# Optimization experiments

Hardware: AMD Instinct MI355X
Metric: run time of the kernel (lower is better)

The kernel has to match this reference:

```python
import jax, jax.numpy as jnp
import numpy as np

B, S, MD, H = 8, 1024, 1024, 16
D = MD // H  # 64
# Faithful to torch: scale = (dim_per_head // num_heads) ** -0.5 (a quirk, not 1/sqrt(D))
SCALE = float((D // H) ** (-0.5))


def setup_inputs() -> dict:
    k0 = jax.random.key(0)
    ks = jax.random.split(k0, 11)
    w = 1.0 / np.sqrt(MD)
    mk = lambda k, shape, s: jax.random.normal(k, shape, dtype=jnp.float32) * s
    return {
        "query": mk(ks[0], (B, S, MD), 1.0),
        "key": mk(ks[1], (B, S, MD), 1.0),
        "value": mk(ks[2], (B, S, MD), 1.0),
        "Wq": mk(ks[3], (MD, MD), w), "bq": mk(ks[4], (MD,), w),
        "Wk": mk(ks[5], (MD, MD), w), "bk": mk(ks[6], (MD,), w),
        "Wv": mk(ks[7], (MD, MD), w), "bv": mk(ks[8], (MD,), w),
        "Wo": mk(ks[9], (MD, MD), w), "bo": mk(ks[10], (MD,), w),
    }


def reference(query, key, value, Wq, bq, Wk, bk, Wv, bv, Wo, bo):
    # Dropout is identity in eval mode (deterministic reference).
    Bq, T, _ = query.shape
    Sk = key.shape[1]
    q = query @ Wq + bq   # [B, T, H*D]
    k = key @ Wk + bk     # [B, S, H*D]
    v = value @ Wv + bv
    # Faithful replication of torch .view(B*H, -1, D): plain row-major reshape
    # (NOT a head transpose -- it chunks sequence/head indices together).
    q = q.reshape(Bq * H, T, D)
    k = k.reshape(Bq * H, Sk, D)
    v = v.reshape(Bq * H, Sk, D)
    attn = jnp.einsum('btd,bsd->bts', q, k) * SCALE          # [B*H, T, S]
    p = jax.nn.softmax(attn, axis=-1)
    ctx = jnp.einsum('bts,bsd->btd', p, v).reshape(Bq, T, H * D)
    output = ctx @ Wo + bo                                    # [B, T, MD]
    a = attn.reshape(Bq, H, T, Sk)
    attn_post = jax.nn.sigmoid(a).sum(axis=1) / H             # [B, T, S]
    return output, attn_post
```

## Files before the change

### kernel.cpp

```cpp
#include <hip/hip_runtime.h>


typedef __attribute__((ext_vector_type(8))) short bf16x8;
typedef __attribute__((ext_vector_type(4))) float f32x4;

static __device__ __forceinline__ short f2bf(float f) {
  union { float f; unsigned u; } v; v.f = f;
  unsigned lsb = (v.u >> 16) & 1u;
  v.u += 0x7fffu + lsb;
  return (short)(v.u >> 16);
}

static __device__ __forceinline__ short f2bf_rhu(float f) {
  union { float f; unsigned u; } v; v.f = f;
  v.u += 0x8000u;
  return (short)(v.u >> 16);
}

static __device__ __forceinline__ float exp2_hw(float x) {
  float r;
  asm("v_exp_f32 %0, %1" : "=v"(r) : "v"(x));
  return r;
}

#define L2E_HALF 0.72134752f

#define GLDS16(gp, lp) __builtin_amdgcn_global_load_lds( \
    (const __attribute__((address_space(1))) void*)(gp), \
    (__attribute__((address_space(3))) void*)(lp), 16, 0, 0)

struct Ptr4 { const float* s[4]; short* d[4]; };
struct Ptr3 { const float* s[3]; short* d[3]; };
struct QkvArgs { const short* A[3]; const short* B[3]; const float* bias[3]; short* C[3]; };

__global__ __launch_bounds__(256) void convt4(Ptr4 a)
{
  const float* __restrict__ src = a.s[blockIdx.z];
  short* __restrict__ dst = a.d[blockIdx.z];
  __shared__ float T[64][65];
  const int tid = threadIdx.x;
  const int c0 = blockIdx.x * 64, r0 = blockIdx.y * 64;
  {
    const int rr = tid >> 4, cc = (tid & 15) * 4;
    for (int i = 0; i < 4; ++i) {
      int row = rr + i * 16;
      const float4 v = *(const float4*)(src + (size_t)(r0 + row) * 1024 + c0 + cc);
      T[row][cc] = v.x; T[row][cc + 1] = v.y; T[row][cc + 2] = v.z; T[row][cc + 3] = v.w;
    }
  }
  __syncthreads();
  {
    const int rr = tid >> 3, cc = (tid & 7) * 8;
    for (int i = 0; i < 2; ++i) {
      int row = rr + i * 32;
      bf16x8 v;
      for (int j = 0; j < 8; ++j) v[j] = f2bf(T[cc + j][row]);
      *(bf16x8*)(dst + (size_t)(c0 + row) * 1024 + r0 + cc) = v;
    }
  }
}

__global__ __launch_bounds__(256) void cvt3(Ptr3 a)
{
  const float* __restrict__ src = a.s[blockIdx.z];
  short* __restrict__ dst = a.d[blockIdx.z];
  const size_t i = ((size_t)blockIdx.x * 256 + threadIdx.x) * 8;
  const float4 v0 = *(const float4*)(src + i);
  const float4 v1 = *(const float4*)(src + i + 4);
  bf16x8 o;
  o[0] = f2bf(v0.x); o[1] = f2bf(v0.y); o[2] = f2bf(v0.z); o[3] = f2bf(v0.w);
  o[4] = f2bf(v1.x); o[5] = f2bf(v1.y); o[6] = f2bf(v1.z); o[7] = f2bf(v1.w);
  *(bf16x8*)(dst + i) = o;
}

__global__ __launch_bounds__(256) void transp_v(
    const short* __restrict__ src, short* __restrict__ dst)
{
  __shared__ short T[64][72];
  const int g = blockIdx.y, t0 = blockIdx.x * 64;
  const short* s = src + (size_t)g * 65536 + (size_t)t0 * 64;
  short* d = dst + (size_t)g * 65536 + t0;
  const int r = threadIdx.x >> 3, c = (threadIdx.x & 7) * 8;
  for (int i = 0; i < 2; ++i) {
    bf16x8 v = *(const bf16x8*)(s + (size_t)(r + i * 32) * 64 + c);
    *(bf16x8*)(&T[r + i * 32][c]) = v;
  }
  __syncthreads();
  for (int i = 0; i < 2; ++i) {
    int dr = r + i * 32;
    bf16x8 v;
    for (int j = 0; j < 8; ++j) v[j] = T[c + j][dr];
    *(bf16x8*)(d + (size_t)dr * 1024 + c) = v;
  }
}

static __device__ __forceinline__ void gemm_body(
    const short* __restrict__ A, const short* __restrict__ BT,
    const float* __restrict__ bias, void* __restrict__ Cp, int mode)
{
  __shared__ short As[128 * 64];
  __shared__ short Bs[128 * 64];
  const int K = 1024, N = 1024;
  const int tid = threadIdx.x;
  const int lane = tid & 63, wave = tid >> 6;
  const int quad = lane >> 4, l16 = lane & 15;
  const int wm = (wave & 1) * 64, wn = (wave >> 1) * 64;
  const int bm = blockIdx.x * 128, bn = blockIdx.y * 128;

  f32x4 acc[4][4] = {};

  const int s_row = tid >> 3;
  const int s_col = (tid & 7) * 8;
  const int lds_base = wave * 512;

  for (int k0 = 0; k0 < K; k0 += 64) {
    for (int i = 0; i < 4; ++i) {
      int row = s_row + i * 32;
      GLDS16(A + (size_t)(bm + row) * K + k0 + s_col, &As[i * 2048 + lds_base]);
      GLDS16(BT + (size_t)(bn + row) * K + k0 + s_col, &Bs[i * 2048 + lds_base]);
    }
    __syncthreads();
    for (int ks = 0; ks < 2; ++ks) {
      bf16x8 af[4], bfr[4];
      for (int mi = 0; mi < 4; ++mi)
        af[mi] = *(const bf16x8*)(&As[(wm + mi * 16 + l16) * 64 + ks * 32 + quad * 8]);
      for (int ni = 0; ni < 4; ++ni)
        bfr[ni] = *(const bf16x8*)(&Bs[(wn + ni * 16 + l16) * 64 + ks * 32 + quad * 8]);
      for (int mi = 0; mi < 4; ++mi)
        for (int ni = 0; ni < 4; ++ni)
          acc[mi][ni] = __builtin_amdgcn_mfma_f32_16x16x32_bf16(af[mi], bfr[ni], acc[mi][ni], 0, 0, 0);
    }
    __syncthreads();
  }

  for (int ni = 0; ni < 4; ++ni) {
    int col = bn + wn + ni * 16 + l16;
    float bv = bias[col];
    for (int mi = 0; mi < 4; ++mi) {
      int row0 = bm + wm + mi * 16 + quad * 4;
      for (int r = 0; r < 4; ++r) {
        int row = row0 + r;
        float fv = acc[mi][ni][r] + bv;
        if (mode == 2) ((float*)Cp)[(size_t)row * N + col] = fv;
        else           ((short*)Cp)[(size_t)row * N + col] = f2bf(fv);
      }
    }
  }
}

__global__ __launch_bounds__(256) void gemm_bt16(
    const short* __restrict__ A, const short* __restrict__ BT,
    const float* __restrict__ bias, void* __restrict__ Cp, int mode)
{
  gemm_body(A, BT, bias, Cp, mode);
}

__global__ __launch_bounds__(256) void gemm_qkv(QkvArgs a)
{
  const int z = blockIdx.z;
  gemm_body(a.A[z], a.B[z], a.bias[z], a.C[z], 0);
}

__global__ __launch_bounds__(256) void attn_fused6(
    const short* __restrict__ Qp, const short* __restrict__ Kp,
    const short* __restrict__ VpT,
    short* __restrict__ ctx,
    float* __restrict__ attn_post)
{
  __shared__ short Plds[16][1032];
  __shared__ float red[16][4];
  __shared__ float ctxred[4][16][64];

  const int tid = threadIdx.x;
  const int wave = tid >> 6, lane = tid & 63;
  const int quad = lane >> 4, l16 = lane & 15;
  const int orig = blockIdx.x;
  const int b = orig & 7;
  const int t0 = (orig >> 3) * 16;
  const int sbase = wave * 256;

  float sig[16][4] = {};

  for (int h = 0; h < 16; ++h) {
    const int g = b * 16 + h;
    const short* Qg = Qp + (size_t)g * 65536;
    const short* Kg = Kp + (size_t)g * 65536;
    const short* Vg = VpT + (size_t)g * 65536;

    bf16x8 aq0 = *(const bf16x8*)(Qg + (t0 + l16) * 64 + quad * 8);
    bf16x8 aq1 = *(const bf16x8*)(Qg + (t0 + l16) * 64 + 32 + quad * 8);

    float sc[16][4];
    float rsum[4] = {0.f, 0.f, 0.f, 0.f};

    bf16x8 kb0[4], kb1[4];
#pragma unroll
    for (int t = 0; t < 4; ++t) {
      int s = sbase + t * 16;
      kb0[t] = *(const bf16x8*)(Kg + (s + l16) * 64 + quad * 8);
      kb1[t] = *(const bf16x8*)(Kg + (s + l16) * 64 + 32 + quad * 8);
    }
#pragma unroll
    for (int tile = 0; tile < 16; ++tile) {
      const int slot = tile & 3;
      bf16x8 bk0 = kb0[slot], bk1 = kb1[slot];
      if (tile < 12) {
        int s = sbase + (tile + 4) * 16;
        kb0[slot] = *(const bf16x8*)(Kg + (s + l16) * 64 + quad * 8);
        kb1[slot] = *(const bf16x8*)(Kg + (s + l16) * 64 + 32 + quad * 8);
      }
      f32x4 c = {0.f, 0.f, 0.f, 0.f};
      c = __builtin_amdgcn_mfma_f32_16x16x32_bf16(aq0, bk0, c, 0, 0, 0);
      c = __builtin_amdgcn_mfma_f32_16x16x32_bf16(aq1, bk1, c, 0, 0, 0);
#pragma unroll
      for (int r = 0; r < 4; ++r) {
        float e = exp2_hw(c[r] * L2E_HALF);
        sc[tile][r] = e;
        rsum[r] += e;
        sig[tile][r] += e * __builtin_amdgcn_rcpf(1.f + e);
      }
    }
#pragma unroll
    for (int r = 0; r < 4; ++r)
      for (int mask = 1; mask < 16; mask <<= 1) rsum[r] += __shfl_xor(rsum[r], mask, 64);
    if (l16 == 0)
      for (int r = 0; r < 4; ++r) red[quad * 4 + r][wave] = rsum[r];
    __syncthreads();
#pragma unroll
    for (int r = 0; r < 4; ++r) {
      int row = quad * 4 + r;
      float s4 = red[row][0] + red[row][1] + red[row][2] + red[row][3];
      float inv = __builtin_amdgcn_rcpf(s4);
#pragma unroll
      for (int tile = 0; tile < 16; ++tile)
        Plds[row][sbase + tile * 16 + l16] = f2bf_rhu(sc[tile][r] * inv);
    }

    f32x4 cacc[4] = {};
    bf16x8 apb[2], vb[2][4];
    apb[0] = *(const bf16x8*)(&Plds[l16][sbase + quad * 8]);
#pragma unroll
    for (int ni = 0; ni < 4; ++ni)
      vb[0][ni] = *(const bf16x8*)(Vg + (ni * 16 + l16) * 1024 + sbase + quad * 8);
#pragma unroll
    for (int ks = 0; ks < 8; ++ks) {
      const int cur = ks & 1, nxt = cur ^ 1;
      if (ks < 7) {
        apb[nxt] = *(const bf16x8*)(&Plds[l16][sbase + (ks + 1) * 32 + quad * 8]);
#pragma unroll
        for (int ni = 0; ni < 4; ++ni)
          vb[nxt][ni] = *(const bf16x8*)(Vg + (ni * 16 + l16) * 1024 + sbase + (ks + 1) * 32 + quad * 8);
      }
#pragma unroll
      for (int ni = 0; ni < 4; ++ni)
        cacc[ni] = __builtin_amdgcn_mfma_f32_16x16x32_bf16(apb[cur], vb[cur][ni], cacc[ni], 0, 0, 0);
    }

    for (int ni = 0; ni < 4; ++ni)
      for (int r = 0; r < 4; ++r)
        ctxred[wave][quad * 4 + r][ni * 16 + l16] = cacc[ni][r];
    __syncthreads();
    short* ctxg = ctx + (size_t)g * 65536 + t0 * 64;
    for (int e = tid; e < 1024; e += 256) {
      int t = e >> 6, dd = e & 63;
      float v = ctxred[0][t][dd] + ctxred[1][t][dd] + ctxred[2][t][dd] + ctxred[3][t][dd];
      ctxg[t * 64 + dd] = f2bf(v);
    }
  }

  float* ap_out = attn_post + (size_t)b * 1048576 + (size_t)t0 * 1024;
  for (int tile = 0; tile < 16; ++tile)
    for (int r = 0; r < 4; ++r)
      ap_out[(quad * 4 + r) * 1024 + sbase + tile * 16 + l16] = sig[tile][r] * 0.0625f;
}

extern "C" void kernel_launch(void* const* d_in, const int* in_sizes, int n_in,
                              void* d_out, int out_size, void* d_ws, size_t ws_size,
                              hipStream_t stream) {
  const float* query = (const float*)d_in[0];
  const float* key   = (const float*)d_in[1];
  const float* value = (const float*)d_in[2];
  const float* Wq = (const float*)d_in[3]; const float* bq = (const float*)d_in[4];
  const float* Wk = (const float*)d_in[5]; const float* bk = (const float*)d_in[6];
  const float* Wv = (const float*)d_in[7]; const float* bv = (const float*)d_in[8];
  const float* Wo = (const float*)d_in[9]; const float* bo = (const float*)d_in[10];

  float* out0 = (float*)d_out;
  float* attn_post = out0 + (8u << 20);

  short* WqT = (short*)d_ws;
  short* WkT = WqT + (1u << 20);
  short* WvT = WkT + (1u << 20);
  short* WoT = WvT + (1u << 20);
  short* Qp  = WoT + (1u << 20);
  short* Kp  = Qp + (8u << 20);
  short* VpT = Kp + (8u << 20);

  dim3 blk(256);
  const size_t NEED_BIG = (size_t)(60u << 20) * 2;

  convt4<<<dim3(16, 16, 4), blk, 0, stream>>>(
      Ptr4{{Wq, Wk, Wv, Wo}, {WqT, WkT, WvT, WoT}});

  short* ctx;
  if (ws_size >= NEED_BIG) {
    short* Xq = VpT + (8u << 20);
    short* Xk = Xq + (8u << 20);
    short* Xv = Xk + (8u << 20);
    short* Vflat = Xv + (8u << 20);
    ctx = Xq;

    cvt3<<<dim3(4096, 1, 3), blk, 0, stream>>>(Ptr3{{query, key, value}, {Xq, Xk, Xv}});
    gemm_qkv<<<dim3(64, 8, 3), blk, 0, stream>>>(
        QkvArgs{{Xq, Xk, Xv}, {WqT, WkT, WvT}, {bq, bk, bv}, {Qp, Kp, Vflat}});
    transp_v<<<dim3(16, 128), blk, 0, stream>>>(Vflat, VpT);
  } else {
    short* Xin = VpT + (8u << 20);
    short* Vflat = Xin + (8u << 20);
    ctx = Xin;

    cvt3<<<dim3(4096, 1, 1), blk, 0, stream>>>(Ptr3{{query, query, query}, {Xin, Xin, Xin}});
    gemm_bt16<<<dim3(64, 8), blk, 0, stream>>>(Xin, WqT, bq, Qp, 0);
    cvt3<<<dim3(4096, 1, 1), blk, 0, stream>>>(Ptr3{{key, key, key}, {Xin, Xin, Xin}});
    gemm_bt16<<<dim3(64, 8), blk, 0, stream>>>(Xin, WkT, bk, Kp, 0);
    cvt3<<<dim3(4096, 1, 1), blk, 0, stream>>>(Ptr3{{value, value, value}, {Xin, Xin, Xin}});
    gemm_bt16<<<dim3(64, 8), blk, 0, stream>>>(Xin, WvT, bv, Vflat, 0);
    transp_v<<<dim3(16, 128), blk, 0, stream>>>(Vflat, VpT);
  }

  attn_fused6<<<dim3(512), blk, 0, stream>>>(Qp, Kp, VpT, ctx, attn_post);
  gemm_bt16<<<dim3(64, 8), blk, 0, stream>>>(ctx, WoT, bo, out0, 2);
}
```

Baseline: 526.7 us.

## Split PV matmul by head-dim across waves, defer softmax normalization

Each wave now computes a 16-column slice of the head dimension over the full key length, instead of a partial sum over a quarter of the keys. This removes the ctxred shared-memory cross-wave reduction and its extra pass. Unnormalized exponentials are written straight into LDS during the score loop, so the sc register array is gone, and the row-sum reciprocal is applied to the context afterwards. Costs: each wave reads the full P row from LDS, and P is rounded to bf16 before normalization, which changes rounding slightly.

```diff
diff --git a/kernel.cpp b/kernel.cpp
--- a/kernel.cpp
+++ b/kernel.cpp
@@ -161,7 +161,7 @@
   gemm_body(a.A[z], a.B[z], a.bias[z], a.C[z], 0);
 }
 
-__global__ __launch_bounds__(256) void attn_fused6(
+__global__ __launch_bounds__(256) void attn_fused7(
     const short* __restrict__ Qp, const short* __restrict__ Kp,
     const short* __restrict__ VpT,
     short* __restrict__ ctx,
@@ -169,7 +169,6 @@
 {
   __shared__ short Plds[16][1032];
   __shared__ float red[16][4];
-  __shared__ float ctxred[4][16][64];
 
   const int tid = threadIdx.x;
   const int wave = tid >> 6, lane = tid & 63;
@@ -190,7 +189,6 @@
     bf16x8 aq0 = *(const bf16x8*)(Qg + (t0 + l16) * 64 + quad * 8);
     bf16x8 aq1 = *(const bf16x8*)(Qg + (t0 + l16) * 64 + 32 + quad * 8);
 
-    float sc[16][4];
     float rsum[4] = {0.f, 0.f, 0.f, 0.f};
 
     bf16x8 kb0[4], kb1[4];
@@ -215,8 +213,8 @@
 #pragma unroll
       for (int r = 0; r < 4; ++r) {
         float e = exp2_hw(c[r] * L2E_HALF);
-        sc[tile][r] = e;
         rsum[r] += e;
+        Plds[quad * 4 + r][sbase + tile * 16 + l16] = f2bf_rhu(e);
         sig[tile][r] += e * __builtin_amdgcn_rcpf(1.f + e);
       }
     }
@@ -226,46 +224,37 @@
     if (l16 == 0)
       for (int r = 0; r < 4; ++r) red[quad * 4 + r][wave] = rsum[r];
     __syncthreads();
+
+    const short* Vw = Vg + (size_t)(wave * 16 + l16) * 1024;
+    f32x4 a0 = {0.f,0.f,0.f,0.f}, a1 = a0, a2 = a0, a3 = a0;
+#pragma unroll
+    for (int sq = 0; sq < 8; ++sq) {
+      bf16x8 p0 = *(const bf16x8*)(&Plds[l16][(sq * 4 + 0) * 32 + quad * 8]);
+      bf16x8 p1 = *(const bf16x8*)(&Plds[l16][(sq * 4 + 1) * 32 + quad * 8]);
+      bf16x8 p2 = *(const bf16x8*)(&Plds[l16][(sq * 4 + 2) * 32 + quad * 8]);
+      bf16x8 p3 = *(const bf16x8*)(&Plds[l16][(sq * 4 + 3) * 32 + quad * 8]);
+      bf16x8 v0 = *(const bf16x8*)(Vw + (sq * 4 + 0) * 32 + quad * 8);
+      bf16x8 v1 = *(const bf16x8*)(Vw + (sq * 4 + 1) * 32 + quad * 8);
+      bf16x8 v2 = *(const bf16x8*)(Vw + (sq * 4 + 2) * 32 + quad * 8);
+      bf16x8 v3 = *(const bf16x8*)(Vw + (sq * 4 + 3) * 32 + quad * 8);
+      a0 = __builtin_amdgcn_mfma_f32_16x16x32_bf16(p0, v0, a0, 0, 0, 0);
+      a1 = __builtin_amdgcn_mfma_f32_16x16x32_bf16(p1, v1, a1, 0, 0, 0);
+      a2 = __builtin_amdgcn_mfma_f32_16x16x32_bf16(p2, v2, a2, 0, 0, 0);
+      a3 = __builtin_amdgcn_mfma_f32_16x16x32_bf16(p3, v3, a3, 0, 0, 0);
+    }
+    f32x4 cacc;
+#pragma unroll
+    for (int r = 0; r < 4; ++r) cacc[r] = (a0[r] + a1[r]) + (a2[r] + a3[r]);
+
+    short* ctxg = ctx + (size_t)g * 65536 + t0 * 64;
 #pragma unroll
     for (int r = 0; r < 4; ++r) {
       int row = quad * 4 + r;
       float s4 = red[row][0] + red[row][1] + red[row][2] + red[row][3];
       float inv = __builtin_amdgcn_rcpf(s4);
-#pragma unroll
-      for (int tile = 0; tile < 16; ++tile)
-        Plds[row][sbase + tile * 16 + l16] = f2bf_rhu(sc[tile][r] * inv);
-    }
-
-    f32x4 cacc[4] = {};
-    bf16x8 apb[2], vb[2][4];
-    apb[0] = *(const bf16x8*)(&Plds[l16][sbase + quad * 8]);
-#pragma unroll
-    for (int ni = 0; ni < 4; ++ni)
-      vb[0][ni] = *(const bf16x8*)(Vg + (ni * 16 + l16) * 1024 + sbase + quad * 8);
-#pragma unroll
-    for (int ks = 0; ks < 8; ++ks) {
-      const int cur = ks & 1, nxt = cur ^ 1;
-      if (ks < 7) {
-        apb[nxt] = *(const bf16x8*)(&Plds[l16][sbase + (ks + 1) * 32 + quad * 8]);
-#pragma unroll
-        for (int ni = 0; ni < 4; ++ni)
-          vb[nxt][ni] = *(const bf16x8*)(Vg + (ni * 16 + l16) * 1024 + sbase + (ks + 1) * 32 + quad * 8);
-      }
-#pragma unroll
-      for (int ni = 0; ni < 4; ++ni)
-        cacc[ni] = __builtin_amdgcn_mfma_f32_16x16x32_bf16(apb[cur], vb[cur][ni], cacc[ni], 0, 0, 0);
-    }
-
-    for (int ni = 0; ni < 4; ++ni)
-      for (int r = 0; r < 4; ++r)
-        ctxred[wave][quad * 4 + r][ni * 16 + l16] = cacc[ni][r];
+      ctxg[row * 64 + wave * 16 + l16] = f2bf(cacc[r] * inv);
+    }
     __syncthreads();
-    short* ctxg = ctx + (size_t)g * 65536 + t0 * 64;
-    for (int e = tid; e < 1024; e += 256) {
-      int t = e >> 6, dd = e & 63;
-      float v = ctxred[0][t][dd] + ctxred[1][t][dd] + ctxred[2][t][dd] + ctxred[3][t][dd];
-      ctxg[t * 64 + dd] = f2bf(v);
-    }
   }
 
   float* ap_out = attn_post + (size_t)b * 1048576 + (size_t)t0 * 1024;
@@ -328,6 +317,6 @@
     transp_v<<<dim3(16, 128), blk, 0, stream>>>(Vflat, VpT);
   }
 
-  attn_fused6<<<dim3(512), blk, 0, stream>>>(Qp, Kp, VpT, ctx, attn_post);
+  attn_fused7<<<dim3(512), blk, 0, stream>>>(Qp, Kp, VpT, ctx, attn_post);
   gemm_bt16<<<dim3(64, 8), blk, 0, stream>>>(ctx, WoT, bo, out0, 2);
 }
```

Result: no change. 526.5 us (-0.1%).
